# Kernel optimization log

Hardware: AMD Instinct MI355X
Metric: run time of the kernel (lower is better)

Reference implementation:

```python
import jax, jax.numpy as jnp
import numpy as np

DIM = 768
NUM_HEADS = 12
HEAD_DIM = DIM // NUM_HEADS
SCALE = HEAD_DIM ** -0.5


def setup_inputs() -> dict:
    key = jax.random.key(0)
    ks = jax.random.split(key, 7)
    B, N = 4, 2048
    s = DIM ** -0.5
    return {
        "x": jax.random.normal(ks[0], (B, N, DIM), dtype=jnp.float32),
        "attn_bias": jax.random.normal(ks[1], (1, NUM_HEADS, N, N), dtype=jnp.float32),
        "Wq": jax.random.normal(ks[2], (DIM, DIM), dtype=jnp.float32) * s,
        "Wk": jax.random.normal(ks[3], (DIM, DIM), dtype=jnp.float32) * s,
        "Wv": jax.random.normal(ks[4], (DIM, DIM), dtype=jnp.float32) * s,
        "Wp": jax.random.normal(ks[5], (DIM, DIM), dtype=jnp.float32) * s,
        "bp": jax.random.normal(ks[6], (DIM,), dtype=jnp.float32) * 0.02,
    }


def reference(x, attn_bias, Wq, Wk, Wv, Wp, bp):
    B, N, C = x.shape
    # Linear layers use y = x @ W.T (torch convention); split heads: [B,H,N,D]
    def heads(y):
        return y.reshape(B, N, NUM_HEADS, HEAD_DIM).transpose(0, 2, 1, 3)
    q = heads(x @ Wq.T)
    k = heads(x @ Wk.T)
    v = heads(x @ Wv.T)
    attn = jnp.einsum("bhnd,bhmd->bhnm", q, k) * SCALE + attn_bias
    attn = jax.nn.softmax(attn, axis=-1)
    out = jnp.einsum("bhnm,bhmd->bhnd", attn, v)
    out = out.transpose(0, 2, 1, 3).reshape(B, N, C)
    return out @ Wp.T + bp
```

## Files before the change

### kernel.cpp

```cpp
#include <hip/hip_runtime.h>
#include <hip/hip_bf16.h>

#define NTOK 2048
#define NHEADS 12
#define HDIM 64
#define DIM 768
#define BATCH 4
#define SCALE_ 0.125f
#define QBLK 64
#define SHIFT_ 16.0f

typedef __attribute__((ext_vector_type(8))) short short8;
typedef __attribute__((ext_vector_type(4))) float f32x4;

__device__ __forceinline__ short f2bf(float f) {
  union { float f; unsigned u; } v; v.f = f;
  unsigned r = v.u + 0x7fffu + ((v.u >> 16) & 1u);
  return (short)(r >> 16);
}

__device__ __forceinline__ f32x4 mfma_bf16(short8 a, short8 b, f32x4 c) {
  return __builtin_amdgcn_mfma_f32_16x16x32_bf16(a, b, c, 0, 0, 0);
}

__device__ __forceinline__ void gload_lds16(const void* g, void* l) {
  __builtin_amdgcn_global_load_lds((const __attribute__((address_space(1))) void*)g,
                                   (__attribute__((address_space(3))) void*)l, 16, 0, 0);
}

__global__ void cvt_x(const float* __restrict__ src, short* __restrict__ dst) {
  int i = blockIdx.x * 256 + threadIdx.x;
  float4 v = ((const float4*)src)[i];
  short4 o; o.x = f2bf(v.x); o.y = f2bf(v.y); o.z = f2bf(v.z); o.w = f2bf(v.w);
  ((short4*)dst)[i] = o;
}

__global__ void cvt_w(const float* __restrict__ w0, const float* __restrict__ w1,
                      const float* __restrict__ w2, const float* __restrict__ w3,
                      short* __restrict__ d0, short* __restrict__ d1,
                      short* __restrict__ d2, short* __restrict__ d3) {
  int i = blockIdx.x * 256 + threadIdx.x;
  const float* s = blockIdx.y == 0 ? w0 : blockIdx.y == 1 ? w1 : blockIdx.y == 2 ? w2 : w3;
  short* d = blockIdx.y == 0 ? d0 : blockIdx.y == 1 ? d1 : blockIdx.y == 2 ? d2 : d3;
  float4 v = ((const float4*)s)[i];
  short4 o; o.x = f2bf(v.x); o.y = f2bf(v.y); o.z = f2bf(v.z); o.w = f2bf(v.w);
  ((short4*)d)[i] = o;
}

__device__ __forceinline__ void gemm_mainloop(const short* __restrict__ A,
                                              const short* __restrict__ B,
                                              int mbase, int nbase,
                                              short* As, short* Bs,
                                              f32x4 (&acc)[4][4], int lane, int w) {
  int lr = lane & 15, lg = lane >> 4;
  int wr = w >> 1, wc = w & 1;
  for (int kb = 0; kb < DIM; kb += 64) {
    if (kb) __syncthreads();
#pragma unroll
    for (int c = 0; c < 4; ++c) {
      int row = w * 32 + c * 8 + (lane >> 3);
      int sch = (lane & 7) ^ (row & 7);
      gload_lds16(A + (size_t)(mbase + row) * DIM + kb + sch * 8, (char*)As + w * 4096 + c * 1024);
      gload_lds16(B + (size_t)(nbase + row) * DIM + kb + sch * 8, (char*)Bs + w * 4096 + c * 1024);
    }
    __syncthreads();
#pragma unroll
    for (int ks = 0; ks < 2; ++ks) {
      short8 af[4], bf[4];
#pragma unroll
      for (int i = 0; i < 4; ++i) {
        int row = wr * 64 + i * 16 + lr;
        int ch = (ks * 4 + lg) ^ (row & 7);
        af[i] = *(const short8*)(As + row * 64 + ch * 8);
      }
#pragma unroll
      for (int j = 0; j < 4; ++j) {
        int row = wc * 64 + j * 16 + lr;
        int ch = (ks * 4 + lg) ^ (row & 7);
        bf[j] = *(const short8*)(Bs + row * 64 + ch * 8);
      }
#pragma unroll
      for (int i = 0; i < 4; ++i)
#pragma unroll
        for (int j = 0; j < 4; ++j)
          acc[i][j] = mfma_bf16(af[i], bf[j], acc[i][j]);
    }
  }
}

__global__ __launch_bounds__(256, 2) void gemm_qkv(const short* __restrict__ xb,
    const short* __restrict__ wq, const short* __restrict__ wk, const short* __restrict__ wv,
    short* __restrict__ Qh, short* __restrict__ Kh, short* __restrict__ Vt) {
  __shared__ __align__(16) short As[128 * 64];
  __shared__ __align__(16) short Bs[128 * 64];
  int nt = blockIdx.x, mt = blockIdx.y, z = blockIdx.z;
  const short* B = z == 0 ? wq : (z == 1 ? wk : wv);
  int tid = threadIdx.x, lane = tid & 63, w = tid >> 6;
  f32x4 acc[4][4] = {};
  gemm_mainloop(xb, B, mt * 128, nt * 128, As, Bs, acc, lane, w);
  int lr = lane & 15, lg = lane >> 4, wr = w >> 1, wc = w & 1;
  if (z < 2) {
    short* dst = z == 0 ? Qh : Kh;
#pragma unroll
    for (int i = 0; i < 4; ++i)
#pragma unroll
      for (int j = 0; j < 4; ++j) {
        int m = mt * 128 + wr * 64 + i * 16 + lg * 4;
        int n = nt * 128 + wc * 64 + j * 16 + lr;
        int bb = m >> 11, nn = m & 2047, hh = n >> 6, d = n & 63;
        size_t base = (((size_t)bb * NHEADS + hh) * NTOK + nn) * HDIM + d;
#pragma unroll
        for (int r = 0; r < 4; ++r)
          dst[base + (size_t)r * HDIM] = f2bf(acc[i][j][r]);
      }
  } else {
#pragma unroll
    for (int i = 0; i < 4; ++i)
#pragma unroll
      for (int j = 0; j < 4; ++j) {
        int m = mt * 128 + wr * 64 + i * 16 + lg * 4;
        int n = nt * 128 + wc * 64 + j * 16 + lr;
        int bb = m >> 11, nn = m & 2047, hh = n >> 6, d = n & 63;
        short4 pk;
        pk.x = f2bf(acc[i][j][0]); pk.y = f2bf(acc[i][j][1]);
        pk.z = f2bf(acc[i][j][2]); pk.w = f2bf(acc[i][j][3]);
        *(short4*)(Vt + (((size_t)bb * NHEADS + hh) * HDIM + d) * NTOK + nn) = pk;
      }
  }
}

__global__ __launch_bounds__(256, 3) void attn_fused(const short* __restrict__ Qh,
    const short* __restrict__ Kh, const short* __restrict__ Vt,
    const float* __restrict__ bias, short* __restrict__ Ob) {
  __shared__ __align__(16) short Ks[2][64 * 64];
  __shared__ __align__(16) short Vs[2][64 * 64];
  __shared__ __align__(16) short Ps[4][16 * 64];
  int d0 = blockIdx.x;
  int wg = (d0 & 7) * 192 + (d0 >> 3);
  int b = wg & 3, qb = (wg >> 2) & 31, h = wg >> 7;
  int tid = threadIdx.x, lane = tid & 63, w = tid >> 6;
  int lr = lane & 15, lg = lane >> 4;

  const short* Q = Qh + ((size_t)b * NHEADS + h) * NTOK * HDIM;
  const short* K = Kh + ((size_t)b * NHEADS + h) * NTOK * HDIM;
  const short* V = Vt + ((size_t)b * NHEADS + h) * HDIM * NTOK;
  const float* Bb = bias + ((size_t)h * NTOK + qb * QBLK + w * 16) * NTOK;

  short8 qf[2];
  {
    const short* qp = Q + (size_t)(qb * QBLK + w * 16 + lr) * HDIM + lg * 8;
    qf[0] = *(const short8*)qp;
    qf[1] = *(const short8*)(qp + 32);
  }

  float psum[4];
#pragma unroll
  for (int r = 0; r < 4; ++r) psum[r] = 0.f;
  f32x4 oacc[4] = {};
  short* myP = (short*)Ps[w];

  auto stage = [&](int buf, int kv) {
#pragma unroll
    for (int c = 0; c < 2; ++c) {
      int row = w * 16 + c * 8 + (lane >> 3);
      int sch = (lane & 7) ^ (row & 7);
      gload_lds16(K + (size_t)(kv + row) * HDIM + sch * 8, (char*)Ks[buf] + w * 2048 + c * 1024);
      gload_lds16(V + (size_t)row * NTOK + kv + sch * 8, (char*)Vs[buf] + w * 2048 + c * 1024);
    }
  };

  auto loadBias = [&](int kv, float (&bv)[4][4]) {
#pragma unroll
    for (int ni = 0; ni < 4; ++ni)
#pragma unroll
      for (int r = 0; r < 4; ++r)
        bv[ni][r] = Bb[(size_t)(lg * 4 + r) * NTOK + kv + ni * 16 + lr] - SHIFT_;
  };

  float bvA[4][4], bvB[4][4];
  loadBias(0, bvA);
  stage(0, 0);
  __syncthreads();

  auto body = [&](int t, int cur, float (&bvc)[4][4], float (&bvn)[4][4]) {
    int kv = t * 64;
    if (t < NTOK / 64 - 1) {
      stage(cur ^ 1, kv + 64);
      loadBias(kv + 64, bvn);
    }

    f32x4 sacc[4];
#pragma unroll
    for (int ni = 0; ni < 4; ++ni) sacc[ni] = (f32x4){0.f, 0.f, 0.f, 0.f};
#pragma unroll
    for (int ni = 0; ni < 4; ++ni) {
      int row = ni * 16 + lr;
      short8 kf0 = *(const short8*)(Ks[cur] + row * 64 + ((lg ^ (row & 7)) * 8));
      short8 kf1 = *(const short8*)(Ks[cur] + row * 64 + (((4 + lg) ^ (row & 7)) * 8));
      sacc[ni] = mfma_bf16(qf[0], kf0, sacc[ni]);
      sacc[ni] = mfma_bf16(qf[1], kf1, sacc[ni]);
    }

#pragma unroll
    for (int ni = 0; ni < 4; ++ni)
#pragma unroll
      for (int r = 0; r < 4; ++r) {
        float p = __expf(fmaf(sacc[ni][r], SCALE_, bvc[ni][r]));
        psum[r] += p;
        int row = lg * 4 + r;
        int col = (ni * 16 + lr) ^ ((row & 7) << 3);
        myP[row * 64 + col] = f2bf(p);
      }

    short8 pf0 = *(const short8*)(myP + lr * 64 + ((lg ^ (lr & 7)) * 8));
    short8 pf1 = *(const short8*)(myP + lr * 64 + (((4 + lg) ^ (lr & 7)) * 8));
#pragma unroll
    for (int ni = 0; ni < 4; ++ni) {
      int row = ni * 16 + lr;
      short8 vf0 = *(const short8*)(Vs[cur] + row * 64 + ((lg ^ (row & 7)) * 8));
      short8 vf1 = *(const short8*)(Vs[cur] + row * 64 + (((4 + lg) ^ (row & 7)) * 8));
      oacc[ni] = mfma_bf16(pf0, vf0, oacc[ni]);
      oacc[ni] = mfma_bf16(pf1, vf1, oacc[ni]);
    }

    __syncthreads();
  };

  for (int t = 0; t < NTOK / 64; t += 2) {
    body(t, 0, bvA, bvB);
    body(t + 1, 1, bvB, bvA);
  }

#pragma unroll
  for (int r = 0; r < 4; ++r) {
    float ps = psum[r];
    ps += __shfl_xor(ps, 1); ps += __shfl_xor(ps, 2);
    ps += __shfl_xor(ps, 4); ps += __shfl_xor(ps, 8);
    float inv = 1.f / ps;
    size_t orow = ((size_t)b * NTOK + qb * QBLK + w * 16 + lg * 4 + r) * DIM + h * HDIM;
#pragma unroll
    for (int ni = 0; ni < 4; ++ni)
      Ob[orow + ni * 16 + lr] = f2bf(oacc[ni][r] * inv);
  }
}

__global__ __launch_bounds__(256, 2) void gemm_proj(const short* __restrict__ Ob,
    const short* __restrict__ wp, const float* __restrict__ bp, float* __restrict__ out) {
  __shared__ __align__(16) short As[128 * 64];
  __shared__ __align__(16) short Bs[128 * 64];
  int nt = blockIdx.x, mt = blockIdx.y;
  int tid = threadIdx.x, lane = tid & 63, w = tid >> 6;
  f32x4 acc[4][4] = {};
  gemm_mainloop(Ob, wp, mt * 128, nt * 128, As, Bs, acc, lane, w);
  int lr = lane & 15, lg = lane >> 4, wr = w >> 1, wc = w & 1;
#pragma unroll
  for (int j = 0; j < 4; ++j) {
    int n = nt * 128 + wc * 64 + j * 16 + lr;
    float bpv = bp[n];
#pragma unroll
    for (int i = 0; i < 4; ++i) {
      int m = mt * 128 + wr * 64 + i * 16 + lg * 4;
#pragma unroll
      for (int r = 0; r < 4; ++r)
        out[(size_t)(m + r) * DIM + n] = acc[i][j][r] + bpv;
    }
  }
}

extern "C" void kernel_launch(void* const* d_in, const int* in_sizes, int n_in,
                              void* d_out, int out_size, void* d_ws, size_t ws_size,
                              hipStream_t stream) {
  const float* x    = (const float*)d_in[0];
  const float* bias = (const float*)d_in[1];
  const float* Wq   = (const float*)d_in[2];
  const float* Wk   = (const float*)d_in[3];
  const float* Wv   = (const float*)d_in[4];
  const float* Wp   = (const float*)d_in[5];
  const float* bp   = (const float*)d_in[6];
  float* out = (float*)d_out;

  char* ws = (char*)d_ws;
  short* xb  = (short*)(ws);
  short* wqb = (short*)(ws + 12582912);
  short* wkb = (short*)(ws + 13762560);
  short* wvb = (short*)(ws + 14942208);
  short* wpb = (short*)(ws + 16121856);
  short* Qh  = (short*)(ws + 17301504);
  short* Kh  = (short*)(ws + 29884416);
  short* Vt  = (short*)(ws + 42467328);
  short* Ob  = (short*)(ws + 55050240);

  cvt_x<<<6144, 256, 0, stream>>>(x, xb);
  cvt_w<<<dim3(576, 4), 256, 0, stream>>>(Wq, Wk, Wv, Wp, wqb, wkb, wvb, wpb);
  gemm_qkv<<<dim3(6, 64, 3), 256, 0, stream>>>(xb, wqb, wkb, wvb, Qh, Kh, Vt);
  attn_fused<<<1536, 256, 0, stream>>>(Qh, Kh, Vt, bias, Ob);
  gemm_proj<<<dim3(6, 64), 256, 0, stream>>>(Ob, wpb, bp, out);
}
```

Before: 212.1 us.

## Transpose QK^T MFMA output for vectorized bias loads, exp2, packed bf16 stores

Swaps the MFMA operand order so each lane holds four consecutive key columns of one query row. That lets the attention bias be read as 16-byte f32x4 vectors instead of scattered scalar loads, and the probabilities be written to LDS as packed pairs. The exponent now uses the hardware v_exp_f32 (exp2) with log2e folded into the scale and bias, and the bf16 conversion uses v_cvt_pk_bf16_f32. It also adds s_setprio around the MFMA phases and raises the occupancy hint to 4, which adds register pressure. The row-sum reduction moves to lane shuffles at the end.

```diff
diff --git a/kernel.cpp b/kernel.cpp
--- a/kernel.cpp
+++ b/kernel.cpp
@@ -6,9 +6,10 @@
 #define HDIM 64
 #define DIM 768
 #define BATCH 4
-#define SCALE_ 0.125f
 #define QBLK 64
-#define SHIFT_ 16.0f
+#define SC2_    0.18033688011112042f
+#define LOG2E_  1.4426950408889634f
+#define SHIFT2_ 23.083120654223415f
 
 typedef __attribute__((ext_vector_type(8))) short short8;
 typedef __attribute__((ext_vector_type(4))) float f32x4;
@@ -26,6 +27,14 @@
 __device__ __forceinline__ void gload_lds16(const void* g, void* l) {
   __builtin_amdgcn_global_load_lds((const __attribute__((address_space(1))) void*)g,
                                    (__attribute__((address_space(3))) void*)l, 16, 0, 0);
+}
+
+__device__ __forceinline__ float exp2_hw(float x) {
+  float r; asm("v_exp_f32 %0, %1" : "=v"(r) : "v"(x)); return r;
+}
+
+__device__ __forceinline__ unsigned cvt_pk_bf16(float lo, float hi) {
+  unsigned r; asm("v_cvt_pk_bf16_f32 %0, %1, %2" : "=v"(r) : "v"(lo), "v"(hi)); return r;
 }
 
 __global__ void cvt_x(const float* __restrict__ src, short* __restrict__ dst) {
@@ -129,7 +138,7 @@
   }
 }
 
-__global__ __launch_bounds__(256, 3) void attn_fused(const short* __restrict__ Qh,
+__global__ __launch_bounds__(256, 4) void attn_fused(const short* __restrict__ Qh,
     const short* __restrict__ Kh, const short* __restrict__ Vt,
     const float* __restrict__ bias, short* __restrict__ Ob) {
   __shared__ __align__(16) short Ks[2][64 * 64];
@@ -144,7 +153,7 @@
   const short* Q = Qh + ((size_t)b * NHEADS + h) * NTOK * HDIM;
   const short* K = Kh + ((size_t)b * NHEADS + h) * NTOK * HDIM;
   const short* V = Vt + ((size_t)b * NHEADS + h) * HDIM * NTOK;
-  const float* Bb = bias + ((size_t)h * NTOK + qb * QBLK + w * 16) * NTOK;
+  const float* Bb = bias + ((size_t)h * NTOK + qb * QBLK + w * 16) * NTOK + (size_t)lr * NTOK;
 
   short8 qf[2];
   {
@@ -153,9 +162,7 @@
     qf[1] = *(const short8*)(qp + 32);
   }
 
-  float psum[4];
-#pragma unroll
-  for (int r = 0; r < 4; ++r) psum[r] = 0.f;
+  float psum = 0.f;
   f32x4 oacc[4] = {};
   short* myP = (short*)Ps[w];
 
@@ -169,20 +176,20 @@
     }
   };
 
-  auto loadBias = [&](int kv, float (&bv)[4][4]) {
-#pragma unroll
-    for (int ni = 0; ni < 4; ++ni)
-#pragma unroll
-      for (int r = 0; r < 4; ++r)
-        bv[ni][r] = Bb[(size_t)(lg * 4 + r) * NTOK + kv + ni * 16 + lr] - SHIFT_;
+  auto loadBias = [&](int kv, f32x4 (&bv)[4]) {
+#pragma unroll
+    for (int ni = 0; ni < 4; ++ni) {
+      f32x4 v = *(const f32x4*)(Bb + kv + ni * 16 + lg * 4);
+      bv[ni] = v * LOG2E_ - SHIFT2_;
+    }
   };
 
-  float bvA[4][4], bvB[4][4];
+  f32x4 bvA[4], bvB[4];
   loadBias(0, bvA);
   stage(0, 0);
   __syncthreads();
 
-  auto body = [&](int t, int cur, float (&bvc)[4][4], float (&bvn)[4][4]) {
+  auto body = [&](int t, int cur, f32x4 (&bvc)[4], f32x4 (&bvn)[4]) {
     int kv = t * 64;
     if (t < NTOK / 64 - 1) {
       stage(cur ^ 1, kv + 64);
@@ -192,28 +199,34 @@
     f32x4 sacc[4];
 #pragma unroll
     for (int ni = 0; ni < 4; ++ni) sacc[ni] = (f32x4){0.f, 0.f, 0.f, 0.f};
+    __builtin_amdgcn_s_setprio(1);
 #pragma unroll
     for (int ni = 0; ni < 4; ++ni) {
       int row = ni * 16 + lr;
       short8 kf0 = *(const short8*)(Ks[cur] + row * 64 + ((lg ^ (row & 7)) * 8));
       short8 kf1 = *(const short8*)(Ks[cur] + row * 64 + (((4 + lg) ^ (row & 7)) * 8));
-      sacc[ni] = mfma_bf16(qf[0], kf0, sacc[ni]);
-      sacc[ni] = mfma_bf16(qf[1], kf1, sacc[ni]);
-    }
-
-#pragma unroll
-    for (int ni = 0; ni < 4; ++ni)
-#pragma unroll
-      for (int r = 0; r < 4; ++r) {
-        float p = __expf(fmaf(sacc[ni][r], SCALE_, bvc[ni][r]));
-        psum[r] += p;
-        int row = lg * 4 + r;
-        int col = (ni * 16 + lr) ^ ((row & 7) << 3);
-        myP[row * 64 + col] = f2bf(p);
-      }
+      sacc[ni] = mfma_bf16(kf0, qf[0], sacc[ni]);
+      sacc[ni] = mfma_bf16(kf1, qf[1], sacc[ni]);
+    }
+    __builtin_amdgcn_s_setprio(0);
+
+#pragma unroll
+    for (int ni = 0; ni < 4; ++ni) {
+      float p0 = exp2_hw(fmaf(sacc[ni][0], SC2_, bvc[ni][0]));
+      float p1 = exp2_hw(fmaf(sacc[ni][1], SC2_, bvc[ni][1]));
+      float p2 = exp2_hw(fmaf(sacc[ni][2], SC2_, bvc[ni][2]));
+      float p3 = exp2_hw(fmaf(sacc[ni][3], SC2_, bvc[ni][3]));
+      psum += (p0 + p1) + (p2 + p3);
+      unsigned w0 = cvt_pk_bf16(p0, p1);
+      unsigned w1 = cvt_pk_bf16(p2, p3);
+      int colb = (ni * 16 + lg * 4) ^ ((lr & 7) << 3);
+      *(unsigned*)(myP + lr * 64 + colb) = w0;
+      *(unsigned*)(myP + lr * 64 + colb + 2) = w1;
+    }
 
     short8 pf0 = *(const short8*)(myP + lr * 64 + ((lg ^ (lr & 7)) * 8));
     short8 pf1 = *(const short8*)(myP + lr * 64 + (((4 + lg) ^ (lr & 7)) * 8));
+    __builtin_amdgcn_s_setprio(1);
 #pragma unroll
     for (int ni = 0; ni < 4; ++ni) {
       int row = ni * 16 + lr;
@@ -222,6 +235,7 @@
       oacc[ni] = mfma_bf16(pf0, vf0, oacc[ni]);
       oacc[ni] = mfma_bf16(pf1, vf1, oacc[ni]);
     }
+    __builtin_amdgcn_s_setprio(0);
 
     __syncthreads();
   };
@@ -231,16 +245,20 @@
     body(t + 1, 1, bvB, bvA);
   }
 
+  float ps = psum;
+  ps += __shfl_xor(ps, 16);
+  ps += __shfl_xor(ps, 32);
+  float inv[4];
+#pragma unroll
+  for (int r = 0; r < 4; ++r)
+    inv[r] = 1.f / __shfl(ps, lg * 4 + r);
+
 #pragma unroll
   for (int r = 0; r < 4; ++r) {
-    float ps = psum[r];
-    ps += __shfl_xor(ps, 1); ps += __shfl_xor(ps, 2);
-    ps += __shfl_xor(ps, 4); ps += __shfl_xor(ps, 8);
-    float inv = 1.f / ps;
     size_t orow = ((size_t)b * NTOK + qb * QBLK + w * 16 + lg * 4 + r) * DIM + h * HDIM;
 #pragma unroll
     for (int ni = 0; ni < 4; ++ni)
-      Ob[orow + ni * 16 + lr] = f2bf(oacc[ni][r] * inv);
+      Ob[orow + ni * 16 + lr] = f2bf(oacc[ni][r] * inv[r]);
   }
 }
 
```

New measurement: 220.4 us. 3.9% more time.
